# Performance work log

Measured on AMD Instinct MI355X. Metric: run time of the kernel, lower is better.

Reference implementation:

```python
import jax, jax.numpy as jnp
import numpy as np
import math

D_IMG = 768
D_TXT = 512
EPS = 1e-5  # torch LayerNorm default


def setup_inputs() -> dict:
    key = jax.random.key(0)
    ks = jax.random.split(key, 12)
    B, N = 256, 197
    s = 0.02
    return {
        "img_feat": jax.random.normal(ks[0], (B, N, D_IMG), jnp.float32),
        "text_global": jax.random.normal(ks[1], (B, D_TXT), jnp.float32),
        # PatchGCN.msg_proj: Linear(D,D) -> GELU -> Linear(D,D)
        "w1_msg": jax.random.normal(ks[2], (D_IMG, D_IMG), jnp.float32) * s,
        "b1_msg": jnp.zeros((D_IMG,), jnp.float32),
        "w2_msg": jax.random.normal(ks[3], (D_IMG, D_IMG), jnp.float32) * s,
        "b2_msg": jnp.zeros((D_IMG,), jnp.float32),
        "gamma_gcn": jnp.ones((1,), jnp.float32),
        # TGSA.text_proj: Linear(512,768) -> GELU -> Linear(768,768)
        "w1_txt": jax.random.normal(ks[4], (D_TXT, D_IMG), jnp.float32) * s,
        "b1_txt": jnp.zeros((D_IMG,), jnp.float32),
        "w2_txt": jax.random.normal(ks[5], (D_IMG, D_IMG), jnp.float32) * s,
        "b2_txt": jnp.zeros((D_IMG,), jnp.float32),
        "ln_w": jnp.ones((D_IMG,), jnp.float32),
        "ln_b": jnp.zeros((D_IMG,), jnp.float32),
        "gamma": jnp.ones((1,), jnp.float32),
    }


def _layernorm(x, w, b):
    mu = jnp.mean(x, axis=-1, keepdims=True)
    var = jnp.mean(jnp.square(x - mu), axis=-1, keepdims=True)
    return (x - mu) * jax.lax.rsqrt(var + EPS) * w + b


def reference(img_feat, text_global, w1_msg, b1_msg, w2_msg, b2_msg, gamma_gcn,
              w1_txt, b1_txt, w2_txt, b2_txt, ln_w, ln_b, gamma):
    D = img_feat.shape[-1]
    cls_token = img_feat[:, 0:1, :]           # [B,1,D]
    x = img_feat[:, 1:, :]                    # [B,Ns,D]

    # PatchGCN: dense patch self-attention message passing
    attn = jnp.einsum("bnd,bmd->bnm", x, x) / math.sqrt(D)
    A = jax.nn.softmax(attn, axis=-1)
    msg = jnp.einsum("bnm,bmd->bnd", A, x)
    h = jax.nn.gelu(msg @ w1_msg + b1_msg, approximate=False)
    msg = h @ w2_msg + b2_msg
    x = x + gamma_gcn * msg

    # Text-conditioned sigmoid gating
    tq = jax.nn.gelu(text_global @ w1_txt + b1_txt, approximate=False) @ w2_txt + b2_txt
    tq = _layernorm(tq, ln_w, ln_b)            # [B,D]
    mask = jax.nn.sigmoid(jnp.einsum("bnd,bd->bn", x, tq))[..., None]  # [B,Ns,1]
    refined = x + gamma * (x * mask)

    return jnp.concatenate([cls_token, refined], axis=1)
```

## Files before the change

kernel.cpp:

```cpp
#include <hip/hip_runtime.h>
#include <hip/hip_bf16.h>


#define BATCH 256
#define NTOK  196
#define PN    256
#define DIMG  768
#define DTXT  512
#define MROWS (BATCH*NTOK)
#define LN_EPS 1e-5f

typedef __hip_bfloat16 bf16_t;
typedef __bf16 bf16x8 __attribute__((ext_vector_type(8)));
typedef float  f32x4  __attribute__((ext_vector_type(4)));

typedef const __attribute__((address_space(1))) void gvoid_t;
typedef __attribute__((address_space(3))) void lvoid_t;

__device__ __forceinline__ float gelu_f(float x){
    return 0.5f * x * (1.0f + erff(x * 0.70710678118654752440f));
}

__global__ void prep_x(const float* __restrict__ img, bf16_t* __restrict__ xb,
                       bf16_t* __restrict__ xt){
    __shared__ float tile[32][33];
    const int b  = blockIdx.z;
    const int m0 = blockIdx.y * 32;
    const int d0 = blockIdx.x * 32;
    const int tx = threadIdx.x, ty = threadIdx.y;
    #pragma unroll
    for (int i = 0; i < 4; i++){
        const int m = m0 + ty + i*8;
        float v = 0.f;
        if (m < NTOK) v = img[((size_t)b*197 + 1 + m)*DIMG + d0 + tx];
        tile[ty + i*8][tx] = v;
        xb[((size_t)b*PN + m)*DIMG + d0 + tx] = __float2bfloat16(v);
    }
    __syncthreads();
    #pragma unroll
    for (int i = 0; i < 4; i++){
        const int d = d0 + ty + i*8;
        xt[((size_t)b*DIMG + d)*PN + m0 + tx] = __float2bfloat16(tile[tx][ty + i*8]);
    }
}

__global__ void prep_w(const float* __restrict__ w, bf16_t* __restrict__ wt){
    __shared__ float tile[32][33];
    const int r0 = blockIdx.y * 32, c0 = blockIdx.x * 32;
    const int tx = threadIdx.x, ty = threadIdx.y;
    #pragma unroll
    for (int i = 0; i < 4; i++)
        tile[ty + i*8][tx] = w[(size_t)(r0 + ty + i*8)*DIMG + c0 + tx];
    __syncthreads();
    #pragma unroll
    for (int i = 0; i < 4; i++)
        wt[(size_t)(c0 + ty + i*8)*DIMG + r0 + tx] = __float2bfloat16(tile[tx][ty + i*8]);
}

__global__ void cls_copy(const float* __restrict__ img, float* __restrict__ out){
    const int i = blockIdx.x * 256 + threadIdx.x;
    const int b = i / DIMG, d = i - b*DIMG;
    out[((size_t)b*197)*DIMG + d] = img[((size_t)b*197)*DIMG + d];
}

__global__ void txt_fc1(const float* __restrict__ text, const float* __restrict__ w,
                        const float* __restrict__ bias, float* __restrict__ h){
    __shared__ float ts[DTXT];
    const int b = blockIdx.y;
    const int n = blockIdx.x * 256 + threadIdx.x;
    for (int k = threadIdx.x; k < DTXT; k += 256) ts[k] = text[(size_t)b*DTXT + k];
    __syncthreads();
    float acc = 0.f;
    for (int k = 0; k < DTXT; k++) acc = fmaf(ts[k], w[(size_t)k*DIMG + n], acc);
    h[(size_t)b*DIMG + n] = gelu_f(acc + bias[n]);
}

__global__ void txt_fc2(const float* __restrict__ h, const float* __restrict__ w,
                        const float* __restrict__ bias, float* __restrict__ tq){
    __shared__ float ts[DIMG];
    const int b = blockIdx.y;
    const int n = blockIdx.x * 256 + threadIdx.x;
    for (int k = threadIdx.x; k < DIMG; k += 256) ts[k] = h[(size_t)b*DIMG + k];
    __syncthreads();
    float acc = 0.f;
    for (int k = 0; k < DIMG; k++) acc = fmaf(ts[k], w[(size_t)k*DIMG + n], acc);
    tq[(size_t)b*DIMG + n] = acc + bias[n];
}

__global__ void txt_ln(float* __restrict__ tq, const float* __restrict__ lw,
                       const float* __restrict__ lb){
    __shared__ float red[4];
    const int b = blockIdx.x, t = threadIdx.x;
    const int wv = t >> 6, lane = t & 63;
    float x[3];
    #pragma unroll
    for (int i = 0; i < 3; i++) x[i] = tq[(size_t)b*DIMG + t + i*256];
    float s = x[0] + x[1] + x[2];
    #pragma unroll
    for (int o = 1; o < 64; o <<= 1) s += __shfl_xor(s, o);
    if (lane == 0) red[wv] = s;
    __syncthreads();
    const float mu = (red[0]+red[1]+red[2]+red[3]) * (1.f/768.f);
    float q = 0.f;
    #pragma unroll
    for (int i = 0; i < 3; i++){ const float d = x[i]-mu; q = fmaf(d, d, q); }
    #pragma unroll
    for (int o = 1; o < 64; o <<= 1) q += __shfl_xor(q, o);
    __syncthreads();
    if (lane == 0) red[wv] = q;
    __syncthreads();
    const float var = (red[0]+red[1]+red[2]+red[3]) * (1.f/768.f);
    const float inv = rsqrtf(var + LN_EPS);
    #pragma unroll
    for (int i = 0; i < 3; i++){
        const int d = t + i*256;
        tq[(size_t)b*DIMG + d] = (x[i]-mu)*inv*lw[d] + lb[d];
    }
}

__global__ void softmax_k(const float* __restrict__ S, bf16_t* __restrict__ A){
    const int gr = blockIdx.x * 4 + (threadIdx.x >> 6);
    const int lane = threadIdx.x & 63;
    if (gr >= MROWS) return;
    const int b = gr / NTOK, m = gr - b*NTOK;
    const float* row = S + ((size_t)b*PN + m)*PN;
    const float scale = 0.03608439182435161256f;
    float v[4]; float mx = -1e30f;
    #pragma unroll
    for (int i = 0; i < 4; i++){
        const int n = lane + i*64;
        const float val = (n < NTOK) ? row[n]*scale : -1e30f;
        v[i] = val; mx = fmaxf(mx, val);
    }
    #pragma unroll
    for (int o = 1; o < 64; o <<= 1) mx = fmaxf(mx, __shfl_xor(mx, o));
    float sum = 0.f;
    #pragma unroll
    for (int i = 0; i < 4; i++){ v[i] = expf(v[i] - mx); sum += v[i]; }
    #pragma unroll
    for (int o = 1; o < 64; o <<= 1) sum += __shfl_xor(sum, o);
    const float inv = 1.f / sum;
    bf16_t* orow = A + ((size_t)b*PN + m)*PN;
    #pragma unroll
    for (int i = 0; i < 4; i++) orow[lane + i*64] = __float2bfloat16(v[i]*inv);
}

__global__ void mask_k(float* __restrict__ out, const float* __restrict__ tq,
                       const float* __restrict__ gam){
    const int gr = blockIdx.x * 4 + (threadIdx.x >> 6);
    const int lane = threadIdx.x & 63;
    if (gr >= MROWS) return;
    const int b = gr / NTOK, n = gr - b*NTOK;
    float* row = out + ((size_t)b*197 + 1 + n)*DIMG;
    const float* t = tq + (size_t)b*DIMG;
    float x[12]; float dot = 0.f;
    #pragma unroll
    for (int i = 0; i < 12; i++){
        x[i] = row[lane + i*64];
        dot = fmaf(x[i], t[lane + i*64], dot);
    }
    #pragma unroll
    for (int o = 1; o < 64; o <<= 1) dot += __shfl_xor(dot, o);
    const float sgm = 1.f / (1.f + expf(-dot));
    const float sc = 1.f + gam[0]*sgm;
    #pragma unroll
    for (int i = 0; i < 12; i++) row[lane + i*64] = x[i]*sc;
}

template<int MODE>
__global__ __launch_bounds__(256) void gemm_bt(
    const bf16_t* __restrict__ Aall, const bf16_t* __restrict__ Btall,
    int lda, int ldb, int K,
    long long strideA, long long strideB,
    float* __restrict__ outF, bf16_t* __restrict__ outB,
    const float* __restrict__ bias, const float* __restrict__ res,
    const float* __restrict__ gscal)
{
    __shared__ __align__(16) bf16_t sA[128*32];
    __shared__ __align__(16) bf16_t sB[128*32];
    const int b  = blockIdx.z;
    const int m0 = blockIdx.y * 128;
    const int n0 = blockIdx.x * 128;
    const bf16_t* Ab = Aall + (long long)b * strideA;
    const bf16_t* Bb = Btall + (long long)b * strideB;

    const int t    = threadIdx.x;
    const int lane = t & 63;
    const int wave = t >> 6;
    const int wm   = (wave & 1) * 64;
    const int wn   = (wave >> 1) * 64;
    const int fr   = lane & 15;
    const int quad = lane >> 4;

    f32x4 acc[4][4];
    #pragma unroll
    for (int i = 0; i < 4; i++)
        #pragma unroll
        for (int j = 0; j < 4; j++)
            acc[i][j] = (f32x4){0.f, 0.f, 0.f, 0.f};

    const int lin0 = t, lin1 = t + 256;
    const int r0 = lin0 >> 2, s0 = (lin0 & 3) * 8;
    const int r1 = lin1 >> 2, s1 = (lin1 & 3) * 8;

    for (int k0 = 0; k0 < K; k0 += 32){
        __syncthreads();
        __builtin_amdgcn_global_load_lds((gvoid_t*)(Ab + (long long)(m0+r0)*lda + k0 + s0),
                                         (lvoid_t*)(sA + lin0*8), 16, 0, 0);
        __builtin_amdgcn_global_load_lds((gvoid_t*)(Ab + (long long)(m0+r1)*lda + k0 + s1),
                                         (lvoid_t*)(sA + lin1*8), 16, 0, 0);
        __builtin_amdgcn_global_load_lds((gvoid_t*)(Bb + (long long)(n0+r0)*ldb + k0 + s0),
                                         (lvoid_t*)(sB + lin0*8), 16, 0, 0);
        __builtin_amdgcn_global_load_lds((gvoid_t*)(Bb + (long long)(n0+r1)*ldb + k0 + s1),
                                         (lvoid_t*)(sB + lin1*8), 16, 0, 0);
        __syncthreads();
        bf16x8 fa[4], fb[4];
        #pragma unroll
        for (int i = 0; i < 4; i++){
            fa[i] = *(const bf16x8*)(sA + (wm + i*16 + fr)*32 + quad*8);
            fb[i] = *(const bf16x8*)(sB + (wn + i*16 + fr)*32 + quad*8);
        }
        #pragma unroll
        for (int i = 0; i < 4; i++)
            #pragma unroll
            for (int j = 0; j < 4; j++)
                acc[i][j] = __builtin_amdgcn_mfma_f32_16x16x32_bf16(fa[i], fb[j], acc[i][j], 0, 0, 0);
    }

    const float g = (MODE == 3) ? gscal[0] : 0.f;
    #pragma unroll
    for (int i = 0; i < 4; i++){
        #pragma unroll
        for (int j = 0; j < 4; j++){
            #pragma unroll
            for (int r = 0; r < 4; r++){
                const int row = m0 + wm + i*16 + quad*4 + r;
                const int col = n0 + wn + j*16 + fr;
                const float v = acc[i][j][r];
                if (MODE == 0){
                    outF[((long long)b*PN + row)*PN + col] = v;
                } else if (MODE == 1){
                    if (row < NTOK)
                        outB[((long long)b*NTOK + row)*DIMG + col] = __float2bfloat16(v);
                } else if (MODE == 2){
                    outB[(long long)row*DIMG + col] = __float2bfloat16(gelu_f(v + bias[col]));
                } else {
                    const int bb = row / NTOK;
                    const int nn = row - bb*NTOK;
                    const long long off = ((long long)bb*197 + 1 + nn)*DIMG + col;
                    outF[off] = res[off] + g*(v + bias[col]);
                }
            }
        }
    }
}

extern "C" void kernel_launch(void* const* d_in, const int* in_sizes, int n_in,
                              void* d_out, int out_size, void* d_ws, size_t ws_size,
                              hipStream_t stream){
    (void)in_sizes; (void)n_in; (void)out_size;
    const float* img  = (const float*)d_in[0];
    const float* text = (const float*)d_in[1];
    const float* w1m  = (const float*)d_in[2];
    const float* b1m  = (const float*)d_in[3];
    const float* w2m  = (const float*)d_in[4];
    const float* b2m  = (const float*)d_in[5];
    const float* ggcn = (const float*)d_in[6];
    const float* w1t  = (const float*)d_in[7];
    const float* b1t  = (const float*)d_in[8];
    const float* w2t  = (const float*)d_in[9];
    const float* b2t  = (const float*)d_in[10];
    const float* lnw  = (const float*)d_in[11];
    const float* lnb  = (const float*)d_in[12];
    const float* gam  = (const float*)d_in[13];
    float* out = (float*)d_out;

    char* p = (char*)d_ws;
    auto alloc = [&](size_t n){ void* r = (void*)p; p += (n + 255) & ~(size_t)255; return r; };
    bf16_t* x_bf   = (bf16_t*)alloc((size_t)BATCH*PN*DIMG*2);
    bf16_t* xT_bf  = (bf16_t*)alloc((size_t)BATCH*DIMG*PN*2);
    float*  S      = (float*) alloc((size_t)BATCH*PN*PN*4);
    bf16_t* A_bf   = (bf16_t*)alloc((size_t)BATCH*PN*PN*2);
    bf16_t* msg_bf = (bf16_t*)alloc((size_t)MROWS*DIMG*2);
    bf16_t* h_bf   = (bf16_t*)alloc((size_t)MROWS*DIMG*2);
    bf16_t* w1T    = (bf16_t*)alloc((size_t)DIMG*DIMG*2);
    bf16_t* w2T    = (bf16_t*)alloc((size_t)DIMG*DIMG*2);
    float*  htxt   = (float*) alloc((size_t)BATCH*DIMG*4);
    float*  tq     = (float*) alloc((size_t)BATCH*DIMG*4);
    if ((size_t)(p - (char*)d_ws) > ws_size) return;

    prep_x<<<dim3(24, 8, BATCH), dim3(32, 8), 0, stream>>>(img, x_bf, xT_bf);
    prep_w<<<dim3(24, 24), dim3(32, 8), 0, stream>>>(w1m, w1T);
    prep_w<<<dim3(24, 24), dim3(32, 8), 0, stream>>>(w2m, w2T);
    cls_copy<<<dim3(768), dim3(256), 0, stream>>>(img, out);
    txt_fc1<<<dim3(3, BATCH), dim3(256), 0, stream>>>(text, w1t, b1t, htxt);
    txt_fc2<<<dim3(3, BATCH), dim3(256), 0, stream>>>(htxt, w2t, b2t, tq);
    txt_ln<<<dim3(BATCH), dim3(256), 0, stream>>>(tq, lnw, lnb);

    gemm_bt<0><<<dim3(2, 2, BATCH), dim3(256), 0, stream>>>(
        x_bf, x_bf, DIMG, DIMG, DIMG,
        (long long)PN*DIMG, (long long)PN*DIMG, S, nullptr, nullptr, nullptr, nullptr);
    softmax_k<<<dim3(MROWS/4), dim3(256), 0, stream>>>(S, A_bf);
    gemm_bt<1><<<dim3(6, 2, BATCH), dim3(256), 0, stream>>>(
        A_bf, xT_bf, PN, PN, PN,
        (long long)PN*PN, (long long)DIMG*PN, nullptr, msg_bf, nullptr, nullptr, nullptr);
    gemm_bt<2><<<dim3(6, 392, 1), dim3(256), 0, stream>>>(
        msg_bf, w1T, DIMG, DIMG, DIMG,
        0, 0, nullptr, h_bf, b1m, nullptr, nullptr);
    gemm_bt<3><<<dim3(6, 392, 1), dim3(256), 0, stream>>>(
        h_bf, w2T, DIMG, DIMG, DIMG,
        0, 0, out, nullptr, b2m, img, ggcn);
    mask_k<<<dim3(MROWS/4), dim3(256), 0, stream>>>(out, tq, gam);
}
```

Before: 881.9 us.

## Precompute sigmoid gate algebraically and fuse it into final GEMM epilogue

```diff
diff --git a/kernel.cpp b/kernel.cpp
--- a/kernel.cpp
+++ b/kernel.cpp
@@ -11,6 +11,7 @@
 #define LN_EPS 1e-5f
 
 typedef __hip_bfloat16 bf16_t;
+typedef __hip_bfloat162 bf2_t;
 typedef __bf16 bf16x8 __attribute__((ext_vector_type(8)));
 typedef float  f32x4  __attribute__((ext_vector_type(4)));
 
@@ -21,13 +22,15 @@
     return 0.5f * x * (1.0f + erff(x * 0.70710678118654752440f));
 }
 
-__global__ void prep_x(const float* __restrict__ img, bf16_t* __restrict__ xb,
-                       bf16_t* __restrict__ xt){
+__global__ void prep_x(const float* __restrict__ img, const float* __restrict__ tq,
+                       bf16_t* __restrict__ xb, bf16_t* __restrict__ xt,
+                       float* __restrict__ dimg){
     __shared__ float tile[32][33];
     const int b  = blockIdx.z;
     const int m0 = blockIdx.y * 32;
     const int d0 = blockIdx.x * 32;
     const int tx = threadIdx.x, ty = threadIdx.y;
+    const float tqv = tq[(size_t)b*DIMG + d0 + tx];
     #pragma unroll
     for (int i = 0; i < 4; i++){
         const int m = m0 + ty + i*8;
@@ -35,6 +38,10 @@
         if (m < NTOK) v = img[((size_t)b*197 + 1 + m)*DIMG + d0 + tx];
         tile[ty + i*8][tx] = v;
         xb[((size_t)b*PN + m)*DIMG + d0 + tx] = __float2bfloat16(v);
+        float p = v * tqv;
+        #pragma unroll
+        for (int o = 1; o < 32; o <<= 1) p += __shfl_xor(p, o);
+        if (tx == 0 && m < NTOK) atomicAdd(&dimg[(size_t)b*NTOK + m], p);
     }
     __syncthreads();
     #pragma unroll
@@ -116,6 +123,19 @@
         const int d = t + i*256;
         tq[(size_t)b*DIMG + d] = (x[i]-mu)*inv*lw[d] + lb[d];
     }
+}
+
+__global__ void calc_u(const float* __restrict__ tq, const bf16_t* __restrict__ w2T,
+                       float* __restrict__ u){
+    __shared__ float ts[DIMG];
+    const int b = blockIdx.y;
+    const int n = blockIdx.x * 256 + threadIdx.x;
+    for (int k = threadIdx.x; k < DIMG; k += 256) ts[k] = tq[(size_t)b*DIMG + k];
+    __syncthreads();
+    float acc = 0.f;
+    for (int k = 0; k < DIMG; k++)
+        acc = fmaf(ts[k], __bfloat162float(w2T[(size_t)k*DIMG + n]), acc);
+    u[(size_t)b*DIMG + n] = acc;
 }
 
 __global__ void softmax_k(const float* __restrict__ S, bf16_t* __restrict__ A){
@@ -145,26 +165,35 @@
     for (int i = 0; i < 4; i++) orow[lane + i*64] = __float2bfloat16(v[i]*inv);
 }
 
-__global__ void mask_k(float* __restrict__ out, const float* __restrict__ tq,
-                       const float* __restrict__ gam){
+__global__ void scale_k(const bf16_t* __restrict__ h, const float* __restrict__ u,
+                        const float* __restrict__ dimg, const float* __restrict__ b2,
+                        const float* __restrict__ tq, const float* __restrict__ ggcn,
+                        const float* __restrict__ gam, float* __restrict__ scale){
     const int gr = blockIdx.x * 4 + (threadIdx.x >> 6);
     const int lane = threadIdx.x & 63;
     if (gr >= MROWS) return;
-    const int b = gr / NTOK, n = gr - b*NTOK;
-    float* row = out + ((size_t)b*197 + 1 + n)*DIMG;
-    const float* t = tq + (size_t)b*DIMG;
-    float x[12]; float dot = 0.f;
-    #pragma unroll
-    for (int i = 0; i < 12; i++){
-        x[i] = row[lane + i*64];
-        dot = fmaf(x[i], t[lane + i*64], dot);
-    }
-    #pragma unroll
-    for (int o = 1; o < 64; o <<= 1) dot += __shfl_xor(dot, o);
-    const float sgm = 1.f / (1.f + expf(-dot));
-    const float sc = 1.f + gam[0]*sgm;
-    #pragma unroll
-    for (int i = 0; i < 12; i++) row[lane + i*64] = x[i]*sc;
+    const int b = gr / NTOK;
+    const bf16_t* hr = h + (size_t)gr*DIMG;
+    const float* ub = u + (size_t)b*DIMG;
+    const float* tb = tq + (size_t)b*DIMG;
+    float s = 0.f;
+    #pragma unroll
+    for (int i = 0; i < 6; i++){
+        const int d = i*128 + lane*2;
+        const bf2_t hv = *(const bf2_t*)(hr + d);
+        const float2 uv = *(const float2*)(ub + d);
+        const float2 bv = *(const float2*)(b2 + d);
+        const float2 tv = *(const float2*)(tb + d);
+        s = fmaf(__bfloat162float(hv.x), uv.x, s);
+        s = fmaf(__bfloat162float(hv.y), uv.y, s);
+        s = fmaf(bv.x, tv.x, s);
+        s = fmaf(bv.y, tv.y, s);
+    }
+    #pragma unroll
+    for (int o = 1; o < 64; o <<= 1) s += __shfl_xor(s, o);
+    const float dot = dimg[gr] + ggcn[0]*s;
+    if (lane == 0)
+        scale[gr] = 1.f + gam[0] / (1.f + expf(-dot));
 }
 
 template<int MODE>
@@ -174,10 +203,12 @@
     long long strideA, long long strideB,
     float* __restrict__ outF, bf16_t* __restrict__ outB,
     const float* __restrict__ bias, const float* __restrict__ res,
-    const float* __restrict__ gscal)
+    const float* __restrict__ gscal, const float* __restrict__ scale)
 {
-    __shared__ __align__(16) bf16_t sA[128*32];
-    __shared__ __align__(16) bf16_t sB[128*32];
+    __shared__ __align__(16) union {
+        struct { bf16_t a[128*32]; bf16_t b[128*32]; } s;
+        float ep[32*132];
+    } sm;
     const int b  = blockIdx.z;
     const int m0 = blockIdx.y * 128;
     const int n0 = blockIdx.x * 128;
@@ -206,19 +237,19 @@
     for (int k0 = 0; k0 < K; k0 += 32){
         __syncthreads();
         __builtin_amdgcn_global_load_lds((gvoid_t*)(Ab + (long long)(m0+r0)*lda + k0 + s0),
-                                         (lvoid_t*)(sA + lin0*8), 16, 0, 0);
+                                         (lvoid_t*)(sm.s.a + lin0*8), 16, 0, 0);
         __builtin_amdgcn_global_load_lds((gvoid_t*)(Ab + (long long)(m0+r1)*lda + k0 + s1),
-                                         (lvoid_t*)(sA + lin1*8), 16, 0, 0);
+                                         (lvoid_t*)(sm.s.a + lin1*8), 16, 0, 0);
         __builtin_amdgcn_global_load_lds((gvoid_t*)(Bb + (long long)(n0+r0)*ldb + k0 + s0),
-                                         (lvoid_t*)(sB + lin0*8), 16, 0, 0);
+                                         (lvoid_t*)(sm.s.b + lin0*8), 16, 0, 0);
         __builtin_amdgcn_global_load_lds((gvoid_t*)(Bb + (long long)(n0+r1)*ldb + k0 + s1),
-                                         (lvoid_t*)(sB + lin1*8), 16, 0, 0);
+                                         (lvoid_t*)(sm.s.b + lin1*8), 16, 0, 0);
         __syncthreads();
         bf16x8 fa[4], fb[4];
         #pragma unroll
         for (int i = 0; i < 4; i++){
-            fa[i] = *(const bf16x8*)(sA + (wm + i*16 + fr)*32 + quad*8);
-            fb[i] = *(const bf16x8*)(sB + (wn + i*16 + fr)*32 + quad*8);
+            fa[i] = *(const bf16x8*)(sm.s.a + (wm + i*16 + fr)*32 + quad*8);
+            fb[i] = *(const bf16x8*)(sm.s.b + (wn + i*16 + fr)*32 + quad*8);
         }
         #pragma unroll
         for (int i = 0; i < 4; i++)
@@ -228,28 +259,78 @@
     }
 
     const float g = (MODE == 3) ? gscal[0] : 0.f;
-    #pragma unroll
-    for (int i = 0; i < 4; i++){
+    const int lr = t >> 3;
+    const int cs = (t & 7) * 16;
+    #pragma unroll
+    for (int c = 0; c < 4; c++){
+        __syncthreads();
+        if ((wm == 0) == (c < 2)){
+            const int ib = (c & 1) * 2;
+            #pragma unroll
+            for (int ii = 0; ii < 2; ii++)
+                #pragma unroll
+                for (int j = 0; j < 4; j++)
+                    #pragma unroll
+                    for (int r = 0; r < 4; r++)
+                        sm.ep[(ii*16 + quad*4 + r)*132 + wn + j*16 + fr] = acc[ib+ii][j][r];
+        }
+        __syncthreads();
+        const int grow = m0 + c*32 + lr;
+        float4 v[4];
+        const float4* vp = (const float4*)(sm.ep + lr*132 + cs);
         #pragma unroll
-        for (int j = 0; j < 4; j++){
+        for (int k = 0; k < 4; k++) v[k] = vp[k];
+
+        if (MODE == 0){
+            float4* dp = (float4*)(outF + ((long long)b*PN + grow)*PN + n0 + cs);
             #pragma unroll
-            for (int r = 0; r < 4; r++){
-                const int row = m0 + wm + i*16 + quad*4 + r;
-                const int col = n0 + wn + j*16 + fr;
-                const float v = acc[i][j][r];
-                if (MODE == 0){
-                    outF[((long long)b*PN + row)*PN + col] = v;
-                } else if (MODE == 1){
-                    if (row < NTOK)
-                        outB[((long long)b*NTOK + row)*DIMG + col] = __float2bfloat16(v);
-                } else if (MODE == 2){
-                    outB[(long long)row*DIMG + col] = __float2bfloat16(gelu_f(v + bias[col]));
-                } else {
-                    const int bb = row / NTOK;
-                    const int nn = row - bb*NTOK;
-                    const long long off = ((long long)bb*197 + 1 + nn)*DIMG + col;
-                    outF[off] = res[off] + g*(v + bias[col]);
+            for (int k = 0; k < 4; k++) dp[k] = v[k];
+        } else if (MODE == 1){
+            if (grow < NTOK){
+                bf16_t tmp[16];
+                #pragma unroll
+                for (int k = 0; k < 4; k++){
+                    tmp[4*k+0] = __float2bfloat16(v[k].x);
+                    tmp[4*k+1] = __float2bfloat16(v[k].y);
+                    tmp[4*k+2] = __float2bfloat16(v[k].z);
+                    tmp[4*k+3] = __float2bfloat16(v[k].w);
                 }
+                float4* dp = (float4*)(outB + ((long long)b*NTOK + grow)*DIMG + n0 + cs);
+                dp[0] = ((float4*)tmp)[0];
+                dp[1] = ((float4*)tmp)[1];
+            }
+        } else if (MODE == 2){
+            const float4* bp = (const float4*)(bias + n0 + cs);
+            bf16_t tmp[16];
+            #pragma unroll
+            for (int k = 0; k < 4; k++){
+                const float4 bv = bp[k];
+                tmp[4*k+0] = __float2bfloat16(gelu_f(v[k].x + bv.x));
+                tmp[4*k+1] = __float2bfloat16(gelu_f(v[k].y + bv.y));
+                tmp[4*k+2] = __float2bfloat16(gelu_f(v[k].z + bv.z));
+                tmp[4*k+3] = __float2bfloat16(gelu_f(v[k].w + bv.w));
+            }
+            float4* dp = (float4*)(outB + (long long)grow*DIMG + n0 + cs);
+            dp[0] = ((float4*)tmp)[0];
+            dp[1] = ((float4*)tmp)[1];
+        } else {
+            const int bb = grow / NTOK;
+            const int nn = grow - bb*NTOK;
+            const long long off = ((long long)bb*197 + 1 + nn)*DIMG + n0 + cs;
+            const float sc = scale[grow];
+            const float4* bp = (const float4*)(bias + n0 + cs);
+            const float4* rp = (const float4*)(res + off);
+            float4* dp = (float4*)(outF + off);
+            #pragma unroll
+            for (int k = 0; k < 4; k++){
+                const float4 bv = bp[k];
+                const float4 rv = rp[k];
+                float4 o;
+                o.x = (rv.x + g*(v[k].x + bv.x)) * sc;
+                o.y = (rv.y + g*(v[k].y + bv.y)) * sc;
+                o.z = (rv.z + g*(v[k].z + bv.z)) * sc;
+                o.w = (rv.w + g*(v[k].w + bv.w)) * sc;
+                dp[k] = o;
             }
         }
     }
@@ -287,28 +368,35 @@
     bf16_t* w2T    = (bf16_t*)alloc((size_t)DIMG*DIMG*2);
     float*  htxt   = (float*) alloc((size_t)BATCH*DIMG*4);
     float*  tq     = (float*) alloc((size_t)BATCH*DIMG*4);
+    float*  u      = (float*) alloc((size_t)BATCH*DIMG*4);
+    float*  dimg   = (float*) alloc((size_t)MROWS*4);
+    float*  scl    = (float*) alloc((size_t)MROWS*4);
     if ((size_t)(p - (char*)d_ws) > ws_size) return;
 
-    prep_x<<<dim3(24, 8, BATCH), dim3(32, 8), 0, stream>>>(img, x_bf, xT_bf);
-    prep_w<<<dim3(24, 24), dim3(32, 8), 0, stream>>>(w1m, w1T);
-    prep_w<<<dim3(24, 24), dim3(32, 8), 0, stream>>>(w2m, w2T);
-    cls_copy<<<dim3(768), dim3(256), 0, stream>>>(img, out);
+    hipMemsetAsync(dimg, 0, (size_t)MROWS*4, stream);
+
     txt_fc1<<<dim3(3, BATCH), dim3(256), 0, stream>>>(text, w1t, b1t, htxt);
     txt_fc2<<<dim3(3, BATCH), dim3(256), 0, stream>>>(htxt, w2t, b2t, tq);
     txt_ln<<<dim3(BATCH), dim3(256), 0, stream>>>(tq, lnw, lnb);
 
+    prep_w<<<dim3(24, 24), dim3(32, 8), 0, stream>>>(w1m, w1T);
+    prep_w<<<dim3(24, 24), dim3(32, 8), 0, stream>>>(w2m, w2T);
+    calc_u<<<dim3(3, BATCH), dim3(256), 0, stream>>>(tq, w2T, u);
+    prep_x<<<dim3(24, 8, BATCH), dim3(32, 8), 0, stream>>>(img, tq, x_bf, xT_bf, dimg);
+    cls_copy<<<dim3(768), dim3(256), 0, stream>>>(img, out);
+
     gemm_bt<0><<<dim3(2, 2, BATCH), dim3(256), 0, stream>>>(
         x_bf, x_bf, DIMG, DIMG, DIMG,
-        (long long)PN*DIMG, (long long)PN*DIMG, S, nullptr, nullptr, nullptr, nullptr);
+        (long long)PN*DIMG, (long long)PN*DIMG, S, nullptr, nullptr, nullptr, nullptr, nullptr);
     softmax_k<<<dim3(MROWS/4), dim3(256), 0, stream>>>(S, A_bf);
     gemm_bt<1><<<dim3(6, 2, BATCH), dim3(256), 0, stream>>>(
         A_bf, xT_bf, PN, PN, PN,
-        (long long)PN*PN, (long long)DIMG*PN, nullptr, msg_bf, nullptr, nullptr, nullptr);
+        (long long)PN*PN, (long long)DIMG*PN, nullptr, msg_bf, nullptr, nullptr, nullptr, nullptr);
     gemm_bt<2><<<dim3(6, 392, 1), dim3(256), 0, stream>>>(
         msg_bf, w1T, DIMG, DIMG, DIMG,
-        0, 0, nullptr, h_bf, b1m, nullptr, nullptr);
+        0, 0, nullptr, h_bf, b1m, nullptr, nullptr, nullptr);
+    scale_k<<<dim3(MROWS/4), dim3(256), 0, stream>>>(h_bf, u, dimg, b2m, tq, ggcn, gam, scl);
     gemm_bt<3><<<dim3(6, 392, 1), dim3(256), 0, stream>>>(
         h_bf, w2T, DIMG, DIMG, DIMG,
-        0, 0, out, nullptr, b2m, img, ggcn);
-    mask_k<<<dim3(MROWS/4), dim3(256), 0, stream>>>(out, tq, gam);
-}
+        0, 0, out, nullptr, b2m, img, ggcn, scl);
+}
```

Result: slower. 928.6 us (+5.3%).
